# Kernel optimization log

Hardware: AMD Instinct MI355X
Metric: run time of the kernel (lower is better)

Reference implementation:

```python
import jax, jax.numpy as jnp
import numpy as np

B, C, H, W = 8, 128, 256, 256
KERNELS = [1, 3, 5]


def _dwconv(x, w, k):
    # depthwise conv, groups == channels, padding k//2 (SAME for odd k)
    return jax.lax.conv_general_dilated(
        x, w, window_strides=(1, 1),
        padding=[(k // 2, k // 2), (k // 2, k // 2)],
        dimension_numbers=("NCHW", "OIHW", "NCHW"),
        feature_group_count=x.shape[1])


def setup_inputs() -> dict:
    key = jax.random.key(0)
    ks = jax.random.split(key, 5)
    x = jax.random.normal(ks[0], (B, C, H, W), jnp.float32)
    # depthwise weights: torch layout [out_ch, in_ch/groups, k, k] = [4C, 1, k, k]
    w1 = jax.random.normal(ks[1], (4 * C, 1, 1, 1), jnp.float32) * 0.2
    w3 = jax.random.normal(ks[2], (4 * C, 1, 3, 3), jnp.float32) * 0.1
    w5 = jax.random.normal(ks[3], (4 * C, 1, 5, 5), jnp.float32) * 0.05
    # proj 1x1 conv: [4C, 12C, 1, 1]
    w_proj = jax.random.normal(ks[4], (4 * C, 12 * C, 1, 1), jnp.float32) * 0.02
    return {"x": x, "w1": w1, "w3": w3, "w5": w5, "w_proj": w_proj}


def reference(x, w1, w3, w5, w_proj):
    # DWT: strided split -> channel concat  [B,C,H,W] -> [B,4C,H/2,W/2]
    xd = jnp.concatenate([
        x[:, :, 0::2, 0::2], x[:, :, 0::2, 1::2],
        x[:, :, 1::2, 0::2], x[:, :, 1::2, 1::2]], axis=1)
    # multi-kernel depthwise convs, concat -> [B,12C,H/2,W/2]
    feats = jnp.concatenate([
        _dwconv(xd, w1, 1), _dwconv(xd, w3, 3), _dwconv(xd, w5, 5)], axis=1)
    # 1x1 projection: [B,12C,h,w] -> [B,4C,h,w]
    y = jnp.einsum("bchw,oc->bohw", feats, w_proj[:, :, 0, 0])
    # IDWT: strided zero-scatter back to [B,C,H,W]
    c = y.shape[1] // 4
    ll, lh, hl, hh = jnp.split(y, 4, axis=1)
    out = jnp.zeros((y.shape[0], c, y.shape[2] * 2, y.shape[3] * 2), y.dtype)
    out = (out.at[:, :, 0::2, 0::2].set(ll)
              .at[:, :, 0::2, 1::2].set(lh)
              .at[:, :, 1::2, 0::2].set(hl)
              .at[:, :, 1::2, 1::2].set(hh))
    return out
```

## Files before the change

kernel.cpp:

```cpp
#include <hip/hip_runtime.h>
#include <hip/hip_bf16.h>
#include <stdint.h>

typedef __bf16 bf16_t;
typedef __bf16 bf16x8 __attribute__((ext_vector_type(8)));
typedef float f32x4 __attribute__((ext_vector_type(4)));

constexpr int CC = 128, HH = 256, WW = 256;
constexpr int C4 = 512, K12 = 1536;
constexpr int AWP_ELEMS = 786432;
constexpr int LW2_ELEMS = 512 * 40;

__global__ __launch_bounds__(256)
void prep(const float* __restrict__ wp, const float* __restrict__ w1,
          const float* __restrict__ w3, const float* __restrict__ w5,
          bf16_t* __restrict__ awp, float* __restrict__ lw2g)
{
    int t = blockIdx.x * 256 + threadIdx.x;
    if (t < AWP_ELEMS) {
        int kk = t & 31, o = (t >> 5) & 511, t2 = t >> 14;
        int g = t2 >> 4, cb = t2 & 15;
        awp[t] = (bf16_t)wp[o * K12 + g * C4 + cb * 32 + kk];
        return;
    }
    int u = t - AWP_ELEMS;
    if (u < LW2_ELEMS) {
        int c4 = u / 40, j = u - c4 * 40;
        int r = j >> 3, v = j & 7;
        float val = 0.f;
        if (v < 5)                 val = w5[c4 * 25 + r * 5 + v];
        else if (r >= 1 && r <= 3) val = w3[c4 * 9 + (r - 1) * 3 + (v - 5)];
        else if (r == 0 && v == 5) val = w1[c4];
        lw2g[u] = val;
    }
}

__device__ __forceinline__ void gload4(const float* g, float* l) {
    __builtin_amdgcn_global_load_lds(
        (const __attribute__((address_space(1))) uint32_t*)g,
        (__attribute__((address_space(3))) uint32_t*)l, 4, 0, 0);
}
__device__ __forceinline__ uint16_t b16bits(float v) {
    return __builtin_bit_cast(uint16_t, (bf16_t)v);
}
__device__ __forceinline__ int btsw(int row) {
    return (((row >> 1) ^ (row >> 2)) & 7) << 4;
}

__global__ __launch_bounds__(512, 4)
void wtconv_mfma(const float* __restrict__ x,
                 const bf16_t* __restrict__ awp,
                 const float* __restrict__ lw2g,
                 float* __restrict__ out)
{
    __shared__ __align__(16) float lx[32][5][68];
    __shared__ __align__(16) char  BtB[2][64 * 256];
    __shared__ __align__(16) float lw2s[32][40];

    const int tid = threadIdx.x;
    const int lane = tid & 63;
    const int wid = __builtin_amdgcn_readfirstlane(tid >> 6);
    const int nb = blockIdx.x;
    const int b = nb & 7;
    const int t = nb >> 3;
    const int i = t >> 1;
    const int half = t & 1;
    const int lrow = lane & 15, lkh = lane >> 4;
    const float* xb = x + (size_t)b * CC * HH * WW;

    for (int e = tid; e < 32 * 5 * 68 / 4; e += 512)
        ((f32x4*)lx)[e] = (f32x4){0.f, 0.f, 0.f, 0.f};
    __syncthreads();

    f32x4 acc[4][4];
#pragma unroll
    for (int a = 0; a < 4; ++a)
#pragma unroll
        for (int c = 0; c < 4; ++c) acc[a][c] = (f32x4){0.f, 0.f, 0.f, 0.f};

    auto issue_own = [&](int kk) {
        const int q4 = kk >> 2, qy = q4 >> 1, qx = q4 & 1;
        const int bcb = (kk & 3) * 32;
#pragma unroll
        for (int cl = 0; cl < 4; ++cl) {
            const int ch = wid * 4 + cl;
#pragma unroll
            for (int r = 0; r < 5; ++r) {
                const int ri = i + r - 2;
                if ((unsigned)ri < 128u) {
                    const float* srow = xb + (((size_t)(bcb + ch)) << 16)
                                      + (2 * ri + qy) * WW + qx;
                    gload4(srow + 2 * (half * 64 + lane), &lx[ch][r][2]);
                    if (lane < 2) {
                        if (half == 0)
                            gload4(srow + 2 * (64 + lane), &lx[ch][r][66]);
                        else
                            gload4(srow + 2 * (62 + lane), &lx[ch][r][0]);
                    }
                }
            }
        }
        const float* wsrc = lw2g + kk * 1280 + wid * 160;
        float* wdst = &lw2s[wid * 4][0];
        gload4(wsrc + lane, wdst);
        gload4(wsrc + 64 + lane, wdst + 64);
        if (lane < 32) gload4(wsrc + 128 + lane, wdst + 128);
    };

    issue_own(0);

    const int chan = tid >> 4;
    const int pxq = tid & 15;
    const int px0 = pxq * 4;

#pragma unroll 1
    for (int k = 0; k <= 16; ++k) {
        __syncthreads();

        if (k < 16) {
            const float* wr = &lw2s[chan][0];
            float f5[4] = {0.f,0.f,0.f,0.f}, f3[4] = {0.f,0.f,0.f,0.f}, f1[4];
            float w1v = 0.f;
#pragma unroll
            for (int r = 0; r < 5; ++r) {
                f32x4 wA = *(const f32x4*)(wr + r * 8);
                f32x4 wB = *(const f32x4*)(wr + r * 8 + 4);
                f32x4 a  = *(const f32x4*)&lx[chan][r][px0];
                f32x4 bv = *(const f32x4*)&lx[chan][r][px0 + 4];
                float c[8] = {a[0],a[1],a[2],a[3],bv[0],bv[1],bv[2],bv[3]};
                if (r == 0) w1v = wB[1];
#pragma unroll
                for (int d = 0; d < 4; ++d)
                    f5[d] += wA[0]*c[d] + wA[1]*c[d+1] + wA[2]*c[d+2]
                           + wA[3]*c[d+3] + wB[0]*c[d+4];
                if (r >= 1 && r <= 3) {
#pragma unroll
                    for (int d = 0; d < 4; ++d)
                        f3[d] += wB[1]*c[d+1] + wB[2]*c[d+2] + wB[3]*c[d+3];
                }
                if (r == 2) {
#pragma unroll
                    for (int d = 0; d < 4; ++d) f1[d] = w1v * c[d + 2];
                }
            }
            char* btb = BtB[k & 1];
            const int cby = chan * 2;
#pragma unroll
            for (int d = 0; d < 4; ++d) {
                const int row = px0 + d;
                const int sw = btsw(row);
                char* base = btb + row * 256;
                *(uint16_t*)(base + ((cby) ^ sw))        = b16bits(f1[d]);
                *(uint16_t*)(base + ((64 + cby) ^ sw))   = b16bits(f3[d]);
                *(uint16_t*)(base + ((128 + cby) ^ sw))  = b16bits(f5[d]);
            }
            if (k < 15) issue_own(k + 1);
        }

        if (k > 0) {
            const int prev = k - 1;
            const char* btb = BtB[prev & 1];
#pragma unroll
            for (int s = 0; s < 3; ++s) {
                bf16x8 bfrag[4];
#pragma unroll
                for (int nf = 0; nf < 4; ++nf) {
                    const int row = nf * 16 + lrow;
                    bfrag[nf] = *(const bf16x8*)(btb + row * 256
                                                 + ((s * 64 + lkh * 16) ^ btsw(row)));
                }
                const bf16_t* abase = awp + (size_t)(s * 16 + prev) * (512 * 32);
                __builtin_amdgcn_s_setprio(1);
#pragma unroll
                for (int mf = 0; mf < 4; ++mf) {
                    const int o = wid * 64 + mf * 16 + lrow;
                    bf16x8 af = *(const bf16x8*)(abase + o * 32 + lkh * 8);
#pragma unroll
                    for (int nf = 0; nf < 4; ++nf)
                        acc[mf][nf] = __builtin_amdgcn_mfma_f32_16x16x32_bf16(
                            af, bfrag[nf], acc[mf][nf], 0, 0, 0);
                }
                __builtin_amdgcn_s_setprio(0);
            }
        }
    }

    const int q = wid >> 1;
    const int oy = 2 * i + (q >> 1), ox = q & 1;
#pragma unroll
    for (int mf = 0; mf < 4; ++mf)
#pragma unroll
        for (int nf = 0; nf < 4; ++nf)
#pragma unroll
            for (int r = 0; r < 4; ++r) {
                const int bco = (wid & 1) * 64 + mf * 16 + lkh * 4 + r;
                const int px  = half * 64 + nf * 16 + lrow;
                out[((size_t)(b * CC + bco) * HH + oy) * WW + 2 * px + ox]
                    = acc[mf][nf][r];
            }
}

extern "C" void kernel_launch(void* const* d_in, const int* in_sizes, int n_in,
                              void* d_out, int out_size, void* d_ws, size_t ws_size,
                              hipStream_t stream) {
    const float* x  = (const float*)d_in[0];
    const float* w1 = (const float*)d_in[1];
    const float* w3 = (const float*)d_in[2];
    const float* w5 = (const float*)d_in[3];
    const float* wp = (const float*)d_in[4];
    float* out = (float*)d_out;
    bf16_t* awp = (bf16_t*)d_ws;
    float* lw2g = (float*)((char*)d_ws + (size_t)AWP_ELEMS * 2);

    int prep_total = AWP_ELEMS + LW2_ELEMS;
    hipLaunchKernelGGL(prep, dim3((prep_total + 255) / 256), dim3(256), 0, stream,
                       wp, w1, w3, w5, awp, lw2g);
    hipLaunchKernelGGL(wtconv_mfma, dim3(2048), dim3(512), 0, stream,
                       x, awp, lw2g, out);
}
```

Before: 520.1 us.

## Split fused conv+GEMM into two kernels staging bf16 features through workspace pages

Replaces the single fused depthwise-conv plus MFMA projection kernel with two kernels. The first computes bf16 depthwise features for a full 128-pixel row and writes them to a global workspace as swizzled pages. The second runs a 1024-thread GEMM that streams those pages into LDS with 16-byte direct global-to-LDS loads, double-buffered, before the MFMA loop. This removes the halo overlap between half-row blocks and lets each stage be tuned on its own, at the cost of writing and re-reading roughly 400 MB of intermediate data through HBM. The old fused path remains as a fallback when the workspace is too small.

```diff
diff --git a/kernel.cpp b/kernel.cpp
--- a/kernel.cpp
+++ b/kernel.cpp
@@ -10,6 +10,12 @@
 constexpr int C4 = 512, K12 = 1536;
 constexpr int AWP_ELEMS = 786432;
 constexpr int LW2_ELEMS = 512 * 40;
+constexpr size_t AWP_BYTES  = (size_t)AWP_ELEMS * 2;
+constexpr size_t LW2_BYTES  = (size_t)LW2_ELEMS * 4;
+constexpr size_t PAGES_OFF  = AWP_BYTES + LW2_BYTES;
+constexpr size_t PAGE_BYTES = 24576;
+constexpr size_t PAGES_BYTES = (size_t)1024 * 16 * PAGE_BYTES;
+constexpr size_t WS_NEEDED  = PAGES_OFF + PAGES_BYTES;
 
 __global__ __launch_bounds__(256)
 void prep(const float* __restrict__ wp, const float* __restrict__ w1,
@@ -40,11 +46,190 @@
         (const __attribute__((address_space(1))) uint32_t*)g,
         (__attribute__((address_space(3))) uint32_t*)l, 4, 0, 0);
 }
+__device__ __forceinline__ void gload16(const char* g, char* l) {
+    __builtin_amdgcn_global_load_lds(
+        (const __attribute__((address_space(1))) uint32_t*)g,
+        (__attribute__((address_space(3))) uint32_t*)l, 16, 0, 0);
+}
 __device__ __forceinline__ uint16_t b16bits(float v) {
     return __builtin_bit_cast(uint16_t, (bf16_t)v);
 }
 __device__ __forceinline__ int btsw(int row) {
     return (((row >> 1) ^ (row >> 2)) & 7) << 4;
+}
+__device__ __forceinline__ int pgf(int px) { return (px ^ (px >> 3)) & 3; }
+
+__global__ __launch_bounds__(512, 2)
+void conv_pages(const float* __restrict__ x, const float* __restrict__ lw2g,
+                char* __restrict__ pages)
+{
+    __shared__ __align__(16) float lx[32][5][136];
+    __shared__ __align__(16) char  Bt[128 * 192];
+    __shared__ __align__(16) float lw2s[32][40];
+
+    const int tid = threadIdx.x;
+    const int lane = tid & 63;
+    const int wid = __builtin_amdgcn_readfirstlane(tid >> 6);
+    const int nb = blockIdx.x;
+    const int b = nb & 7, i = nb >> 3;
+    const float* xb = x + (size_t)b * CC * HH * WW;
+    char* pbase = pages + (size_t)((b * 128 + i) * 16) * PAGE_BYTES;
+
+    for (int e = tid; e < 32 * 5 * 136 / 4; e += 512)
+        ((f32x4*)lx)[e] = (f32x4){0.f, 0.f, 0.f, 0.f};
+    __syncthreads();
+
+    auto issue_own = [&](int kk) {
+        const int q4 = kk >> 2, qy = q4 >> 1, qx = q4 & 1;
+        const int bcb = (kk & 3) * 32;
+#pragma unroll
+        for (int cl = 0; cl < 4; ++cl) {
+            const int ch = wid * 4 + cl;
+#pragma unroll
+            for (int r = 0; r < 5; ++r) {
+                const int ri = i + r - 2;
+                if ((unsigned)ri < 128u) {
+                    const float* s = xb + (((size_t)(bcb + ch)) << 16)
+                                   + (2 * ri + qy) * WW + qx;
+                    gload4(s + 2 * lane,       &lx[ch][r][2]);
+                    gload4(s + 128 + 2 * lane, &lx[ch][r][66]);
+                }
+            }
+        }
+        const float* wsrc = lw2g + kk * 1280 + wid * 160;
+        float* wdst = &lw2s[wid * 4][0];
+        gload4(wsrc + lane, wdst);
+        gload4(wsrc + 64 + lane, wdst + 64);
+        if (lane < 32) gload4(wsrc + 128 + lane, wdst + 128);
+    };
+    issue_own(0);
+
+    const int chan = tid >> 4;
+    const int px0 = (tid & 15) * 8;
+    const int c2lo = (chan * 2) & 15;
+    const int chunk = chan >> 3;
+
+#pragma unroll 1
+    for (int cb = 0; cb < 16; ++cb) {
+        __syncthreads();
+
+        const float* wr = &lw2s[chan][0];
+        float f5[8] = {0,0,0,0,0,0,0,0}, f3[8] = {0,0,0,0,0,0,0,0}, f1[8];
+        float w1v = 0.f;
+#pragma unroll
+        for (int r = 0; r < 5; ++r) {
+            f32x4 wA = *(const f32x4*)(wr + r * 8);
+            f32x4 wB = *(const f32x4*)(wr + r * 8 + 4);
+            f32x4 v0 = *(const f32x4*)&lx[chan][r][px0];
+            f32x4 v1 = *(const f32x4*)&lx[chan][r][px0 + 4];
+            f32x4 v2 = *(const f32x4*)&lx[chan][r][px0 + 8];
+            float cc[12] = {v0[0],v0[1],v0[2],v0[3], v1[0],v1[1],v1[2],v1[3],
+                            v2[0],v2[1],v2[2],v2[3]};
+            if (r == 0) w1v = wB[1];
+#pragma unroll
+            for (int d = 0; d < 8; ++d)
+                f5[d] += wA[0]*cc[d] + wA[1]*cc[d+1] + wA[2]*cc[d+2]
+                       + wA[3]*cc[d+3] + wB[0]*cc[d+4];
+            if (r >= 1 && r <= 3) {
+#pragma unroll
+                for (int d = 0; d < 8; ++d)
+                    f3[d] += wB[1]*cc[d+1] + wB[2]*cc[d+2] + wB[3]*cc[d+3];
+            }
+            if (r == 2) {
+#pragma unroll
+                for (int d = 0; d < 8; ++d) f1[d] = w1v * cc[d + 2];
+            }
+        }
+#pragma unroll
+        for (int d = 0; d < 8; ++d) {
+            const int row = px0 + d;
+            char* base = Bt + row * 192;
+            const int ck = (((chunk ^ pgf(row)) & 3) << 4) + c2lo;
+            *(uint16_t*)(base + ck)        = b16bits(f1[d]);
+            *(uint16_t*)(base + 64 + ck)   = b16bits(f3[d]);
+            *(uint16_t*)(base + 128 + ck)  = b16bits(f5[d]);
+        }
+        if (cb < 15) issue_own(cb + 1);
+        __syncthreads();
+        char* dst = pbase + (size_t)cb * PAGE_BYTES;
+        for (int e = tid; e < 1536; e += 512)
+            *(f32x4*)(dst + e * 16) = *(const f32x4*)(Bt + e * 16);
+    }
+}
+
+__global__ __launch_bounds__(1024, 4)
+void gemm_pages(const bf16_t* __restrict__ awp, const char* __restrict__ pages,
+                float* __restrict__ out)
+{
+    __shared__ __align__(16) char pg[2][24576];
+
+    const int tid = threadIdx.x;
+    const int lane = tid & 63;
+    const int wid = __builtin_amdgcn_readfirstlane(tid >> 6);
+    const int nb = blockIdx.x;
+    const int b = nb & 7, i = nb >> 3;
+    const int wm = wid & 7, wn = wid >> 3;
+    const int lrow = lane & 15, lkh = lane >> 4;
+    const char* pbase = pages + (size_t)((b * 128 + i) * 16) * PAGE_BYTES;
+
+    f32x4 acc[4][4];
+#pragma unroll
+    for (int a = 0; a < 4; ++a)
+#pragma unroll
+        for (int c = 0; c < 4; ++c) acc[a][c] = (f32x4){0.f, 0.f, 0.f, 0.f};
+
+    auto stage = [&](int cb) {
+        const char* src = pbase + (size_t)cb * PAGE_BYTES;
+        char* dst = pg[cb & 1];
+#pragma unroll 1
+        for (int t = wid; t < 24; t += 16)
+            gload16(src + t * 1024 + lane * 16, dst + t * 1024);
+    };
+    stage(0);
+
+#pragma unroll 1
+    for (int cb = 0; cb < 16; ++cb) {
+        __syncthreads();
+        if (cb < 15) stage(cb + 1);
+
+        const char* p = pg[cb & 1];
+#pragma unroll
+        for (int g = 0; g < 3; ++g) {
+            bf16x8 bfrag[4];
+#pragma unroll
+            for (int nf = 0; nf < 4; ++nf) {
+                const int px = wn * 64 + nf * 16 + lrow;
+                bfrag[nf] = *(const bf16x8*)(p + px * 192 + g * 64
+                                + (((lkh ^ pgf(px)) & 3) << 4));
+            }
+            const bf16_t* abase = awp + (size_t)(g * 16 + cb) * (512 * 32);
+            __builtin_amdgcn_s_setprio(1);
+#pragma unroll
+            for (int mf = 0; mf < 4; ++mf) {
+                const int o = wm * 64 + mf * 16 + lrow;
+                bf16x8 af = *(const bf16x8*)(abase + o * 32 + lkh * 8);
+#pragma unroll
+                for (int nf = 0; nf < 4; ++nf)
+                    acc[mf][nf] = __builtin_amdgcn_mfma_f32_16x16x32_bf16(
+                        af, bfrag[nf], acc[mf][nf], 0, 0, 0);
+            }
+            __builtin_amdgcn_s_setprio(0);
+        }
+    }
+
+    const int q = wm >> 1;
+    const int oy = 2 * i + (q >> 1), ox = q & 1;
+#pragma unroll
+    for (int mf = 0; mf < 4; ++mf)
+#pragma unroll
+        for (int nf = 0; nf < 4; ++nf)
+#pragma unroll
+            for (int r = 0; r < 4; ++r) {
+                const int bco = (wm & 1) * 64 + mf * 16 + lkh * 4 + r;
+                const int px  = wn * 64 + nf * 16 + lrow;
+                out[((size_t)(b * CC + bco) * HH + oy) * WW + 2 * px + ox]
+                    = acc[mf][nf][r];
+            }
 }
 
 __global__ __launch_bounds__(512, 4)
@@ -106,7 +291,6 @@
         gload4(wsrc + 64 + lane, wdst + 64);
         if (lane < 32) gload4(wsrc + 128 + lane, wdst + 128);
     };
-
     issue_own(0);
 
     const int chan = tid >> 4;
@@ -209,12 +393,21 @@
     const float* w5 = (const float*)d_in[3];
     const float* wp = (const float*)d_in[4];
     float* out = (float*)d_out;
-    bf16_t* awp = (bf16_t*)d_ws;
-    float* lw2g = (float*)((char*)d_ws + (size_t)AWP_ELEMS * 2);
+    bf16_t* awp  = (bf16_t*)d_ws;
+    float*  lw2g = (float*)((char*)d_ws + AWP_BYTES);
+    char*   pages = (char*)d_ws + PAGES_OFF;
 
     int prep_total = AWP_ELEMS + LW2_ELEMS;
     hipLaunchKernelGGL(prep, dim3((prep_total + 255) / 256), dim3(256), 0, stream,
                        wp, w1, w3, w5, awp, lw2g);
-    hipLaunchKernelGGL(wtconv_mfma, dim3(2048), dim3(512), 0, stream,
-                       x, awp, lw2g, out);
-}
+
+    if (ws_size >= WS_NEEDED) {
+        hipLaunchKernelGGL(conv_pages, dim3(1024), dim3(512), 0, stream,
+                           x, lw2g, pages);
+        hipLaunchKernelGGL(gemm_pages, dim3(1024), dim3(1024), 0, stream,
+                           awp, pages, out);
+    } else {
+        hipLaunchKernelGGL(wtconv_mfma, dim3(2048), dim3(512), 0, stream,
+                           x, awp, lw2g, out);
+    }
+}
```

New measurement: 669.0 us. 1.29x slower.
